# Kernel tuning notes

Hardware: AMD Instinct MI355X
Metric: run time of the kernel (lower is better)

The kernel has to match this reference:

```python
import jax, jax.numpy as jnp
import numpy as np

NUM_HEADS = 16
ROPE_BASE = 10000.0
EPS = 1e-6


def _rms_norm(x, scale):
    # RMSNorm over last dim with learnable scale (QKNorm over full `dim`).
    var = jnp.mean(jnp.square(x), axis=-1, keepdims=True)
    return x * jax.lax.rsqrt(var + EPS) * scale


def _rotate_half(x):
    x1, x2 = jnp.split(x, 2, axis=-1)
    return jnp.concatenate([-x2, x1], axis=-1)


def _apply_rope(q, k, rotary_dim):
    # q, k: (b, n, h, d); rotate first rotary_dim channels of each head.
    n = q.shape[1]
    half = rotary_dim // 2
    inv_freq = 1.0 / (ROPE_BASE ** (jnp.arange(0, half, dtype=jnp.float32) * 2.0 / rotary_dim))
    freqs = jnp.arange(n, dtype=jnp.float32)[:, None] * inv_freq[None, :]  # (n, half)
    emb = jnp.concatenate([freqs, freqs], axis=-1)  # (n, rotary_dim)
    cos = jnp.cos(emb)[None, :, None, :]
    sin = jnp.sin(emb)[None, :, None, :]

    def rot(x):
        x_rot, x_pass = x[..., :rotary_dim], x[..., rotary_dim:]
        x_rot = x_rot * cos + _rotate_half(x_rot) * sin
        return jnp.concatenate([x_rot, x_pass], axis=-1)

    return rot(q), rot(k)


def setup_inputs() -> dict:
    key = jax.random.key(0)
    ks = jax.random.split(key, 7)
    input_dim, dim = 1024, 1024
    b, n = 2, 2048
    s_in = 1.0 / np.sqrt(input_dim)
    s_d = 1.0 / np.sqrt(dim)
    return {
        "input": jax.random.normal(ks[0], (b, n, input_dim), dtype=jnp.float32),
        "w_qkv": jax.random.normal(ks[1], (input_dim, 3 * dim), dtype=jnp.float32) * s_in,
        "b_qkv": jax.random.normal(ks[2], (3 * dim,), dtype=jnp.float32) * 0.01,
        "q_scale": jnp.ones((dim,), dtype=jnp.float32) + 0.01 * jax.random.normal(ks[3], (dim,)),
        "k_scale": jnp.ones((dim,), dtype=jnp.float32) + 0.01 * jax.random.normal(ks[4], (dim,)),
        "w_out": jax.random.normal(ks[5], (dim, input_dim), dtype=jnp.float32) * s_d,
        "b_out": jax.random.normal(ks[6], (input_dim,), dtype=jnp.float32) * 0.01,
    }


def reference(input, w_qkv, b_qkv, q_scale, k_scale, w_out, b_out):
    b, n, _ = input.shape
    h = NUM_HEADS
    qkv = input @ w_qkv + b_qkv  # (b, n, 3*dim)
    q, k, v = jnp.split(qkv, 3, axis=-1)
    q = _rms_norm(q, q_scale)
    k = _rms_norm(k, k_scale)
    d = q.shape[-1] // h
    q = q.reshape(b, n, h, d)
    k = k.reshape(b, n, h, d)
    v = v.reshape(b, n, h, d)
    q, k = _apply_rope(q, k, rotary_dim=d)  # partial_rotary_factor=1
    scale = d ** (-0.5)
    attn = jnp.einsum("bqhd,bkhd->bhqk", q, k) * scale
    attn = jax.nn.softmax(attn, axis=-1)
    out = jnp.einsum("bhqk,bkhd->bqhd", attn, v).reshape(b, n, h * d)
    return out @ w_out + b_out
```

## Files before the change

kernel.cpp:

```cpp
#include <hip/hip_runtime.h>
#include <stdint.h>

typedef short bf16x8 __attribute__((ext_vector_type(8)));
typedef float f32x4 __attribute__((ext_vector_type(4)));
typedef float f32x16 __attribute__((ext_vector_type(16)));
typedef unsigned short u16;

#define MFMA_BF16 __builtin_amdgcn_mfma_f32_16x16x32_bf16
#define MFMA32 __builtin_amdgcn_mfma_f32_32x32x16_bf16
#define LOG2E 1.44269504088896f

#if __has_builtin(__builtin_amdgcn_exp2f)
#define EXP2(x) __builtin_amdgcn_exp2f(x)
#else
#define EXP2(x) exp2f(x)
#endif

static __device__ __forceinline__ u16 f2bf(float x) {
  union { float f; unsigned u; } v; v.f = x;
  unsigned r = v.u + 0x7fffu + ((v.u >> 16) & 1u);
  return (u16)(r >> 16);
}
static __device__ __forceinline__ float bf2f(u16 h) {
  union { unsigned u; float f; } v; v.u = ((unsigned)h) << 16; return v.f;
}
static __device__ __forceinline__ unsigned cvt_pk_bf16(float lo, float hi) {
  unsigned r;
  asm("v_cvt_pk_bf16_f32 %0, %1, %2" : "=v"(r) : "v"(lo), "v"(hi));
  return r;
}
static __device__ __forceinline__ void gld_lds16(const u16* g, u16* l) {
  __builtin_amdgcn_global_load_lds(
      (const __attribute__((address_space(1))) void*)g,
      (__attribute__((address_space(3))) void*)l, 16, 0, 0);
}

__global__ __launch_bounds__(256) void k_cast(const float* __restrict__ x,
                                              u16* __restrict__ y) {
  int i = blockIdx.x * 256 + threadIdx.x;
  const float4* p = (const float4*)x;
  float4 a = p[i * 2], b = p[i * 2 + 1];
  ushort4 o0, o1;
  o0.x = f2bf(a.x); o0.y = f2bf(a.y); o0.z = f2bf(a.z); o0.w = f2bf(a.w);
  o1.x = f2bf(b.x); o1.y = f2bf(b.y); o1.z = f2bf(b.z); o1.w = f2bf(b.w);
  ushort4* q = (ushort4*)y;
  q[i * 2] = o0; q[i * 2 + 1] = o1;
}

__global__ __launch_bounds__(256) void k_wtrans(const float* __restrict__ w,
                                                u16* __restrict__ wt,
                                                int K, int N) {
  int n = blockIdx.x * 256 + threadIdx.x;
  int k0 = blockIdx.y * 8;
  if (n >= N) return;
  u16 o[8];
#pragma unroll
  for (int j = 0; j < 8; j++) o[j] = f2bf(w[(size_t)(k0 + j) * N + n]);
  *(uint4*)&wt[(size_t)n * K + k0] = *(const uint4*)o;
}

template <int OUT_BF16>
__global__ __launch_bounds__(256, 2) void k_gemm(const u16* __restrict__ A,
                                                 const u16* __restrict__ Bt,
                                                 const float* __restrict__ bias,
                                                 void* __restrict__ Cp,
                                                 int M, int N, int K) {
  __shared__ u16 As[128 * 64];
  __shared__ u16 Bs[128 * 64];
  const int tid = threadIdx.x;
  const int lane = tid & 63;
  const int wid = tid >> 6;
  const int wm = wid >> 1, wn = wid & 1;
  const int m0 = blockIdx.x * 128, n0 = blockIdx.y * 128;

  const int sr = tid >> 3;
  const int sc = tid & 7;
  const int scsw = sc ^ (sr & 7);
  const u16* ga = A + (size_t)(m0 + sr) * K + (scsw << 3);
  const u16* gb = Bt + (size_t)(n0 + sr) * K + (scsw << 3);

  const int ar = wm * 64 + (lane & 15);
  const int br = wn * 64 + (lane & 15);
  const int cs0 = lane >> 4;

  f32x4 acc[4][4] = {};

  for (int k0 = 0; k0 < K; k0 += 64) {
    __syncthreads();
#pragma unroll
    for (int i = 0; i < 4; i++)
      gld_lds16(ga + k0 + i * (32 * K), &As[((tid & ~63) + 256 * i) * 8]);
#pragma unroll
    for (int i = 0; i < 4; i++)
      gld_lds16(gb + k0 + i * (32 * K), &Bs[((tid & ~63) + 256 * i) * 8]);
    __syncthreads();
#pragma unroll
    for (int kk = 0; kk < 2; kk++) {
      bf16x8 af[4], bfr[4];
#pragma unroll
      for (int mi = 0; mi < 4; mi++)
        af[mi] = *(const bf16x8*)&As[(ar + mi * 16) * 64 +
                                     (((kk * 4 + cs0) ^ (ar & 7)) << 3)];
#pragma unroll
      for (int ni = 0; ni < 4; ni++)
        bfr[ni] = *(const bf16x8*)&Bs[(br + ni * 16) * 64 +
                                      (((kk * 4 + cs0) ^ (br & 7)) << 3)];
#pragma unroll
      for (int mi = 0; mi < 4; mi++)
#pragma unroll
        for (int ni = 0; ni < 4; ni++)
          acc[mi][ni] = MFMA_BF16(af[mi], bfr[ni], acc[mi][ni], 0, 0, 0);
    }
  }

  const int crow0 = m0 + wm * 64 + ((lane >> 4) << 2);
  const int ccol0 = n0 + wn * 64 + (lane & 15);
#pragma unroll
  for (int ni = 0; ni < 4; ni++) {
    float bv = bias[ccol0 + ni * 16];
#pragma unroll
    for (int mi = 0; mi < 4; mi++) {
#pragma unroll
      for (int r = 0; r < 4; r++) {
        float v = acc[mi][ni][r] + bv;
        size_t idx = (size_t)(crow0 + mi * 16 + r) * N + ccol0 + ni * 16;
        if (OUT_BF16) ((u16*)Cp)[idx] = f2bf(v);
        else ((float*)Cp)[idx] = v;
      }
    }
  }
}

__global__ __launch_bounds__(256) void k_normrope(const u16* __restrict__ qkv,
                                                  const float* __restrict__ qscale,
                                                  const float* __restrict__ kscale,
                                                  u16* __restrict__ Qb,
                                                  u16* __restrict__ Kb) {
  const int row = blockIdx.x;
  const int b = row >> 11, n = row & 2047;
  const int t = threadIdx.x;
  __shared__ float qn[1024], kn[1024];
  __shared__ float csb[32], snb[32];
  __shared__ float redq[4], redk[4];

  ushort4 q4 = *(const ushort4*)&qkv[(size_t)row * 3072 + t * 4];
  ushort4 k4 = *(const ushort4*)&qkv[(size_t)row * 3072 + 1024 + t * 4];
  float qv[4] = {bf2f(q4.x), bf2f(q4.y), bf2f(q4.z), bf2f(q4.w)};
  float kv[4] = {bf2f(k4.x), bf2f(k4.y), bf2f(k4.z), bf2f(k4.w)};
  float sq = 0.f, sk = 0.f;
#pragma unroll
  for (int j = 0; j < 4; j++) { sq += qv[j] * qv[j]; sk += kv[j] * kv[j]; }
#pragma unroll
  for (int o = 1; o < 64; o <<= 1) {
    sq += __shfl_xor(sq, o);
    sk += __shfl_xor(sk, o);
  }
  if ((t & 63) == 0) { redq[t >> 6] = sq; redk[t >> 6] = sk; }
  if (t < 32) {
    float inv = exp2f(-(float)t * (13.287712379549449f / 32.f));
    float fr = (float)n * inv;
    float s, c;
    sincosf(fr, &s, &c);
    csb[t] = c; snb[t] = s;
  }
  __syncthreads();
  float rq = rsqrtf((redq[0] + redq[1] + redq[2] + redq[3]) * (1.f / 1024.f) + 1e-6f);
  float rk = rsqrtf((redk[0] + redk[1] + redk[2] + redk[3]) * (1.f / 1024.f) + 1e-6f);
#pragma unroll
  for (int j = 0; j < 4; j++) {
    int jj = t * 4 + j;
    qn[jj] = qv[j] * rq * qscale[jj];
    kn[jj] = kv[j] * rk * kscale[jj];
  }
  __syncthreads();
  const int j0 = t * 4;
  const int h = j0 >> 6;
  const int d0 = j0 & 63;
  u16 qo[4], ko[4];
#pragma unroll
  for (int j = 0; j < 4; j++) {
    int jj = j0 + j;
    int dd = d0 + j;
    float c = csb[dd & 31], s = snb[dd & 31];
    float oq, ok;
    if (dd < 32) {
      oq = qn[jj] * c - qn[jj + 32] * s;
      ok = kn[jj] * c - kn[jj + 32] * s;
    } else {
      oq = qn[jj] * c + qn[jj - 32] * s;
      ok = kn[jj] * c + kn[jj - 32] * s;
    }
    qo[j] = f2bf(oq * (0.125f * LOG2E));
    ko[j] = f2bf(ok);
  }
  const size_t base = ((size_t)(b * 16 + h) * 2048 + n) * 64 + d0;
  *(ushort4*)&Qb[base] = *(const ushort4*)qo;
  *(ushort4*)&Kb[base] = *(const ushort4*)ko;
}

__global__ __launch_bounds__(256) void k_vtrans(const u16* __restrict__ qkv,
                                                u16* __restrict__ Vt) {
  const int bh = blockIdx.y;
  const int b = bh >> 4, h = bh & 15;
  const int n0 = blockIdx.x * 64;
  const int t = threadIdx.x;
  __shared__ u16 tile[64][72];
#pragma unroll
  for (int i = 0; i < 2; i++) {
    int r = (t >> 3) + 32 * i;
    int c = t & 7;
    uint4 v = *(const uint4*)&qkv[((size_t)(b * 2048 + n0 + r)) * 3072 + 2048 + h * 64 + c * 8];
    *(uint4*)&tile[r][c * 8] = v;
  }
  __syncthreads();
#pragma unroll
  for (int i = 0; i < 2; i++) {
    int dr = (t >> 3) + 32 * i;
    int c = t & 7;
    u16 vals[8];
#pragma unroll
    for (int j = 0; j < 8; j++) vals[j] = tile[c * 8 + j][dr];
    *(uint4*)&Vt[((size_t)bh * 64 + dr) * 2048 + n0 + c * 8] = *(const uint4*)vals;
  }
}

__global__ __launch_bounds__(512, 4) void k_attn(const u16* __restrict__ Qb,
                                                 const u16* __restrict__ Kb,
                                                 const u16* __restrict__ Vt,
                                                 u16* __restrict__ Ob) {
  const int bh = blockIdx.y;
  const int q0 = blockIdx.x * 128;
  const int t = threadIdx.x, lane = t & 63, wid = t >> 6;
  const int grp = wid >> 2, sub = wid & 3;
  const int q = lane & 31, hi = lane >> 5;

  __shared__ u16 smem[32768];
  u16* Ks = smem;
  u16* Vs = smem + 4 * 4096;

  const u16* Qg = Qb + (size_t)bh * 2048 * 64;
  const u16* Kg = Kb + (size_t)bh * 2048 * 64;
  const u16* Vg = Vt + (size_t)bh * 64 * 2048;

  bf16x8 qf[4];
  {
    const u16* qrow = Qg + (size_t)(q0 + sub * 32 + q) * 64;
#pragma unroll
    for (int kk = 0; kk < 4; kk++)
      qf[kk] = *(const bf16x8*)&qrow[kk * 16 + hi * 8];
  }

  f32x16 ot[2] = {};
  float lacc[4] = {0.f, 0.f, 0.f, 0.f};

  const int srow = t >> 3;
  const int sslot = (t & 7) ^ (srow & 7);
  const u16* gk = Kg + srow * 64 + (sslot << 3);
  const u16* gv = Vg + (size_t)srow * 2048 + (sslot << 3);
  const int ldoff = (t & ~63) * 8;

#define STAGE(tile)                                                     \
  do {                                                                  \
    gld_lds16(gk + (size_t)(tile) * 4096, &Ks[((tile) & 3) * 4096 + ldoff]); \
    gld_lds16(gv + (size_t)(tile) * 64,   &Vs[((tile) & 3) * 4096 + ldoff]); \
  } while (0)

  STAGE(0); STAGE(1); STAGE(2); STAGE(3);

  for (int s = 0; s < 16; ++s) {
    if (s < 15) asm volatile("s_waitcnt vmcnt(4)" ::: "memory");
    else        asm volatile("s_waitcnt vmcnt(0)" ::: "memory");
    asm volatile("s_barrier" ::: "memory");

    const int myt = 2 * s + grp;
    const u16* Kc = &Ks[(myt & 3) * 4096];
    const u16* Vc = &Vs[(myt & 3) * 4096];

    f32x16 sv0 = {}, sv1 = {};
#pragma unroll
    for (int kk = 0; kk < 4; kk++) {
      const int kr0 = 0 * 32 + q;
      const int kr1 = 1 * 32 + q;
      bf16x8 kf0 = *(const bf16x8*)&Kc[kr0 * 64 + (((kk * 2 + hi) ^ (kr0 & 7)) << 3)];
      bf16x8 kf1 = *(const bf16x8*)&Kc[kr1 * 64 + (((kk * 2 + hi) ^ (kr1 & 7)) << 3)];
      __builtin_amdgcn_s_setprio(1);
      sv0 = MFMA32(kf0, qf[kk], sv0, 0, 0, 0);
      sv1 = MFMA32(kf1, qf[kk], sv1, 0, 0, 0);
      __builtin_amdgcn_s_setprio(0);
    }

    unsigned w[2][8];
#pragma unroll
    for (int i = 0; i < 8; i++) {
      float p0 = EXP2(sv0[2 * i]);
      float p1 = EXP2(sv0[2 * i + 1]);
      lacc[i & 3] += p0 + p1;
      w[0][i] = cvt_pk_bf16(p0, p1);
    }
#pragma unroll
    for (int i = 0; i < 8; i++) {
      float p0 = EXP2(sv1[2 * i]);
      float p1 = EXP2(sv1[2 * i + 1]);
      lacc[i & 3] += p0 + p1;
      w[1][i] = cvt_pk_bf16(p0, p1);
    }

#pragma unroll
    for (int ks = 0; ks < 4; ks++) {
      const int kvt = ks >> 1, i0 = (ks & 1) * 4;
      unsigned xs0 = hi ? w[kvt][i0 + 0] : w[kvt][i0 + 2];
      unsigned xs1 = hi ? w[kvt][i0 + 1] : w[kvt][i0 + 3];
      unsigned y0 = __shfl_xor(xs0, 32);
      unsigned y1 = __shfl_xor(xs1, 32);
      union { unsigned u[4]; bf16x8 v; } pf;
      pf.u[0] = hi ? y0 : w[kvt][i0 + 0];
      pf.u[1] = hi ? y1 : w[kvt][i0 + 1];
      pf.u[2] = hi ? w[kvt][i0 + 2] : y0;
      pf.u[3] = hi ? w[kvt][i0 + 3] : y1;
#pragma unroll
      for (int dt = 0; dt < 2; dt++) {
        const int vr = dt * 32 + q;
        bf16x8 va = *(const bf16x8*)&Vc[vr * 64 + (((ks * 2 + hi) ^ (vr & 7)) << 3)];
        __builtin_amdgcn_s_setprio(1);
        ot[dt] = MFMA32(va, pf.v, ot[dt], 0, 0, 0);
        __builtin_amdgcn_s_setprio(0);
      }
    }

    asm volatile("s_barrier" ::: "memory");
    if (s < 14) { STAGE(2 * s + 4); STAGE(2 * s + 5); }
  }
#undef STAGE

  float lsum = (lacc[0] + lacc[1]) + (lacc[2] + lacc[3]);

  lsum += __shfl_xor(lsum, 32);
  __syncthreads();
  float* obuf = (float*)smem;
  float* lbuf = (float*)(smem + 16384);
  if (grp == 1) {
    float* ob = obuf + (sub * 32 + q) * 64;
#pragma unroll
    for (int dt = 0; dt < 2; dt++)
#pragma unroll
      for (int g = 0; g < 4; g++) {
        float4 v4 = {ot[dt][4 * g], ot[dt][4 * g + 1], ot[dt][4 * g + 2], ot[dt][4 * g + 3]};
        *(float4*)&ob[dt * 32 + 8 * g + 4 * hi] = v4;
      }
    if (hi == 0) lbuf[sub * 32 + q] = lsum;
  }
  __syncthreads();
  if (grp == 0) {
    const float* ob = obuf + (sub * 32 + q) * 64;
    const float invl = 1.f / (lsum + lbuf[sub * 32 + q]);
    const int b = bh >> 4, h = bh & 15;
    const int rowq = q0 + sub * 32 + q;
    u16* orow = Ob + (size_t)(b * 2048 + rowq) * 1024 + h * 64;
#pragma unroll
    for (int dt = 0; dt < 2; dt++)
#pragma unroll
      for (int g = 0; g < 4; g++) {
        float4 v4 = *(const float4*)&ob[dt * 32 + 8 * g + 4 * hi];
        u16 o4[4];
        o4[0] = f2bf((ot[dt][4 * g + 0] + v4.x) * invl);
        o4[1] = f2bf((ot[dt][4 * g + 1] + v4.y) * invl);
        o4[2] = f2bf((ot[dt][4 * g + 2] + v4.z) * invl);
        o4[3] = f2bf((ot[dt][4 * g + 3] + v4.w) * invl);
        *(ushort4*)&orow[dt * 32 + 8 * g + 4 * hi] = *(const ushort4*)o4;
      }
  }
}

extern "C" void kernel_launch(void* const* d_in, const int* in_sizes, int n_in,
                              void* d_out, int out_size, void* d_ws, size_t ws_size,
                              hipStream_t stream) {
  const float* input = (const float*)d_in[0];
  const float* w_qkv = (const float*)d_in[1];
  const float* b_qkv = (const float*)d_in[2];
  const float* q_scale = (const float*)d_in[3];
  const float* k_scale = (const float*)d_in[4];
  const float* w_out = (const float*)d_in[5];
  const float* b_out = (const float*)d_in[6];
  float* out = (float*)d_out;

  char* ws = (char*)d_ws;
  u16* Abuf  = (u16*)(ws);
  u16* WqkvT = (u16*)(ws + 8388608);
  u16* WoutT = (u16*)(ws + 14680064);
  u16* qkv   = (u16*)(ws + 16777216);
  u16* Qb    = (u16*)(ws + 41943040);
  u16* Kb    = (u16*)(ws + 50331648);
  u16* Vt    = (u16*)(ws + 58720256);
  u16* Attn  = (u16*)(ws + 67108864);

  k_cast<<<2048, 256, 0, stream>>>(input, Abuf);
  k_wtrans<<<dim3(12, 128), 256, 0, stream>>>(w_qkv, WqkvT, 1024, 3072);
  k_wtrans<<<dim3(4, 128), 256, 0, stream>>>(w_out, WoutT, 1024, 1024);
  k_gemm<1><<<dim3(32, 24), 256, 0, stream>>>(Abuf, WqkvT, b_qkv, qkv, 4096, 3072, 1024);
  k_normrope<<<4096, 256, 0, stream>>>(qkv, q_scale, k_scale, Qb, Kb);
  k_vtrans<<<dim3(32, 32), 256, 0, stream>>>(qkv, Vt);
  k_attn<<<dim3(16, 32), 512, 0, stream>>>(Qb, Kb, Vt, Attn);
  k_gemm<0><<<dim3(32, 8), 256, 0, stream>>>(Attn, WoutT, b_out, out, 4096, 1024, 1024);
}
```

Before: 131.0 us.

## Double-buffer GEMM LDS loads and precompute RoPE cos/sin table

The GEMM kernel now keeps two LDS buffers and prefetches k-tile kt+2 while computing kt, waiting with explicit vmcnt and barriers instead of a full sync before every tile. This aims to hide global-to-LDS load latency behind MFMA work. Launch bounds rise to 3 blocks per CU even though LDS use doubles to 64KB per block, so the occupancy hint may not be reachable. Separately, RoPE cos/sin values are precomputed once into a table by a new kernel, so normrope no longer runs sincos per row.

```diff
diff --git a/kernel.cpp b/kernel.cpp
--- a/kernel.cpp
+++ b/kernel.cpp
@@ -59,14 +59,25 @@
   *(uint4*)&wt[(size_t)n * K + k0] = *(const uint4*)o;
 }
 
+__global__ __launch_bounds__(256) void k_ropetab(float2* __restrict__ tab) {
+  int i = blockIdx.x * 256 + threadIdx.x;
+  int n = i >> 5, f = i & 31;
+  float inv = exp2f(-(float)f * (13.287712379549449f / 32.f));
+  float fr = (float)n * inv;
+  float s, c;
+  sincosf(fr, &s, &c);
+  float2 cs; cs.x = c; cs.y = s;
+  tab[i] = cs;
+}
+
 template <int OUT_BF16>
-__global__ __launch_bounds__(256, 2) void k_gemm(const u16* __restrict__ A,
+__global__ __launch_bounds__(256, 3) void k_gemm(const u16* __restrict__ A,
                                                  const u16* __restrict__ Bt,
                                                  const float* __restrict__ bias,
                                                  void* __restrict__ Cp,
                                                  int M, int N, int K) {
-  __shared__ u16 As[128 * 64];
-  __shared__ u16 Bs[128 * 64];
+  __shared__ u16 As[2][128 * 64];
+  __shared__ u16 Bs[2][128 * 64];
   const int tid = threadIdx.x;
   const int lane = tid & 63;
   const int wid = tid >> 6;
@@ -84,26 +95,40 @@
   const int cs0 = lane >> 4;
 
   f32x4 acc[4][4] = {};
-
-  for (int k0 = 0; k0 < K; k0 += 64) {
-    __syncthreads();
-#pragma unroll
-    for (int i = 0; i < 4; i++)
-      gld_lds16(ga + k0 + i * (32 * K), &As[((tid & ~63) + 256 * i) * 8]);
-#pragma unroll
-    for (int i = 0; i < 4; i++)
-      gld_lds16(gb + k0 + i * (32 * K), &Bs[((tid & ~63) + 256 * i) * 8]);
-    __syncthreads();
+  const int nk = K >> 6;
+
+#define GSTAGE(kt, buf)                                                      \
+  do {                                                                       \
+    _Pragma("unroll")                                                        \
+    for (int i = 0; i < 4; i++)                                              \
+      gld_lds16(ga + (kt) * 64 + i * (32 * K),                               \
+                &As[buf][((tid & ~63) + 256 * i) * 8]);                      \
+    _Pragma("unroll")                                                        \
+    for (int i = 0; i < 4; i++)                                              \
+      gld_lds16(gb + (kt) * 64 + i * (32 * K),                               \
+                &Bs[buf][((tid & ~63) + 256 * i) * 8]);                      \
+  } while (0)
+
+  GSTAGE(0, 0);
+  GSTAGE(1, 1);
+
+  for (int kt = 0; kt < nk; ++kt) {
+    if (kt < nk - 1) asm volatile("s_waitcnt vmcnt(8)" ::: "memory");
+    else             asm volatile("s_waitcnt vmcnt(0)" ::: "memory");
+    asm volatile("s_barrier" ::: "memory");
+
+    const u16* Ac = As[kt & 1];
+    const u16* Bc = Bs[kt & 1];
 #pragma unroll
     for (int kk = 0; kk < 2; kk++) {
       bf16x8 af[4], bfr[4];
 #pragma unroll
       for (int mi = 0; mi < 4; mi++)
-        af[mi] = *(const bf16x8*)&As[(ar + mi * 16) * 64 +
+        af[mi] = *(const bf16x8*)&Ac[(ar + mi * 16) * 64 +
                                      (((kk * 4 + cs0) ^ (ar & 7)) << 3)];
 #pragma unroll
       for (int ni = 0; ni < 4; ni++)
-        bfr[ni] = *(const bf16x8*)&Bs[(br + ni * 16) * 64 +
+        bfr[ni] = *(const bf16x8*)&Bc[(br + ni * 16) * 64 +
                                       (((kk * 4 + cs0) ^ (br & 7)) << 3)];
 #pragma unroll
       for (int mi = 0; mi < 4; mi++)
@@ -111,7 +136,11 @@
         for (int ni = 0; ni < 4; ni++)
           acc[mi][ni] = MFMA_BF16(af[mi], bfr[ni], acc[mi][ni], 0, 0, 0);
     }
-  }
+
+    asm volatile("s_barrier" ::: "memory");
+    if (kt + 2 < nk) GSTAGE(kt + 2, kt & 1);
+  }
+#undef GSTAGE
 
   const int crow0 = m0 + wm * 64 + ((lane >> 4) << 2);
   const int ccol0 = n0 + wn * 64 + (lane & 15);
@@ -134,13 +163,13 @@
 __global__ __launch_bounds__(256) void k_normrope(const u16* __restrict__ qkv,
                                                   const float* __restrict__ qscale,
                                                   const float* __restrict__ kscale,
+                                                  const float2* __restrict__ tab,
                                                   u16* __restrict__ Qb,
                                                   u16* __restrict__ Kb) {
   const int row = blockIdx.x;
   const int b = row >> 11, n = row & 2047;
   const int t = threadIdx.x;
   __shared__ float qn[1024], kn[1024];
-  __shared__ float csb[32], snb[32];
   __shared__ float redq[4], redk[4];
 
   ushort4 q4 = *(const ushort4*)&qkv[(size_t)row * 3072 + t * 4];
@@ -156,12 +185,14 @@
     sk += __shfl_xor(sk, o);
   }
   if ((t & 63) == 0) { redq[t >> 6] = sq; redk[t >> 6] = sk; }
-  if (t < 32) {
-    float inv = exp2f(-(float)t * (13.287712379549449f / 32.f));
-    float fr = (float)n * inv;
-    float s, c;
-    sincosf(fr, &s, &c);
-    csb[t] = c; snb[t] = s;
+
+  const int j0 = t * 4;
+  const int d0 = j0 & 63;
+  float2 cs[4];
+  {
+    const float2* tb = tab + n * 32 + (d0 & 31);
+    *(float4*)&cs[0] = *(const float4*)&tb[0];
+    *(float4*)&cs[2] = *(const float4*)&tb[2];
   }
   __syncthreads();
   float rq = rsqrtf((redq[0] + redq[1] + redq[2] + redq[3]) * (1.f / 1024.f) + 1e-6f);
@@ -173,15 +204,13 @@
     kn[jj] = kv[j] * rk * kscale[jj];
   }
   __syncthreads();
-  const int j0 = t * 4;
   const int h = j0 >> 6;
-  const int d0 = j0 & 63;
   u16 qo[4], ko[4];
 #pragma unroll
   for (int j = 0; j < 4; j++) {
     int jj = j0 + j;
     int dd = d0 + j;
-    float c = csb[dd & 31], s = snb[dd & 31];
+    float c = cs[j].x, s = cs[j].y;
     float oq, ok;
     if (dd < 32) {
       oq = qn[jj] * c - qn[jj + 32] * s;
@@ -279,8 +308,8 @@
     f32x16 sv0 = {}, sv1 = {};
 #pragma unroll
     for (int kk = 0; kk < 4; kk++) {
-      const int kr0 = 0 * 32 + q;
-      const int kr1 = 1 * 32 + q;
+      const int kr0 = q;
+      const int kr1 = 32 + q;
       bf16x8 kf0 = *(const bf16x8*)&Kc[kr0 * 64 + (((kk * 2 + hi) ^ (kr0 & 7)) << 3)];
       bf16x8 kf1 = *(const bf16x8*)&Kc[kr1 * 64 + (((kk * 2 + hi) ^ (kr1 & 7)) << 3)];
       __builtin_amdgcn_s_setprio(1);
@@ -333,7 +362,6 @@
 #undef STAGE
 
   float lsum = (lacc[0] + lacc[1]) + (lacc[2] + lacc[3]);
-
   lsum += __shfl_xor(lsum, 32);
   __syncthreads();
   float* obuf = (float*)smem;
@@ -392,12 +420,14 @@
   u16* Kb    = (u16*)(ws + 50331648);
   u16* Vt    = (u16*)(ws + 58720256);
   u16* Attn  = (u16*)(ws + 67108864);
+  float2* Rt = (float2*)(ws + 75497472);
 
   k_cast<<<2048, 256, 0, stream>>>(input, Abuf);
   k_wtrans<<<dim3(12, 128), 256, 0, stream>>>(w_qkv, WqkvT, 1024, 3072);
   k_wtrans<<<dim3(4, 128), 256, 0, stream>>>(w_out, WoutT, 1024, 1024);
+  k_ropetab<<<256, 256, 0, stream>>>(Rt);
   k_gemm<1><<<dim3(32, 24), 256, 0, stream>>>(Abuf, WqkvT, b_qkv, qkv, 4096, 3072, 1024);
-  k_normrope<<<4096, 256, 0, stream>>>(qkv, q_scale, k_scale, Qb, Kb);
+  k_normrope<<<4096, 256, 0, stream>>>(qkv, q_scale, k_scale, Rt, Qb, Kb);
   k_vtrans<<<dim3(32, 32), 256, 0, stream>>>(qkv, Vt);
   k_attn<<<dim3(16, 32), 512, 0, stream>>>(Qb, Kb, Vt, Attn);
   k_gemm<0><<<dim3(32, 8), 256, 0, stream>>>(Attn, WoutT, b_out, out, 4096, 1024, 1024);
```

After: 138.4 us. 1.06x slower.
